# Performance work log

Hardware: AMD Instinct MI355X
Metric: run time of the kernel (lower is better)

## Reference

```python
import jax, jax.numpy as jnp
import numpy as np

NEG = float(-2**32 + 1)  # huge negative used by the original sign-based masking
EPS = 1e-8
NUM_BLOCKS = 3
NUM_HEADS = 1


def _mha(xq, xk, xv, Wq, bq, Wk, bk, Wv, bv):
    # manual QKV with ReLU, as in the torch module
    Q = jax.nn.relu(xq @ Wq + bq)   # [B, Lq, D]
    K = jax.nn.relu(xk @ Wk + bk)   # [B, Lk, D]
    V = jax.nn.relu(xv @ Wv + bv)
    B, Lq, D = Q.shape
    Lk = K.shape[1]
    dh = D // NUM_HEADS
    Qh = Q.reshape(B, Lq, NUM_HEADS, dh)
    Kh = K.reshape(B, Lk, NUM_HEADS, dh)
    Vh = V.reshape(B, Lk, NUM_HEADS, dh)
    scores = jnp.einsum('bqhd,bkhd->bhqk', Qh, Kh) / jnp.sqrt(jnp.float32(dh))
    # sign-based key padding mask (rows whose embedding-sum is exactly 0)
    key_mask0 = (jnp.sign(jnp.abs(jnp.sum(xk, axis=-1))) == 0.0).astype(scores.dtype)  # [B, Lk]
    cond = key_mask0[:, None, None, :]
    scores = NEG * cond + scores * (1.0 - cond)
    attn = jax.nn.softmax(scores, axis=-1)
    # post-softmax query mask
    qmask = jnp.sign(jnp.abs(jnp.sum(xq, axis=-1)))  # [B, Lq]
    attn = attn * qmask[:, None, :, None]
    out = jnp.einsum('bhqk,bkhd->bqhd', attn, Vh).reshape(B, Lq, D)
    return out + xq  # residual; note: the torch mha never applies its layernorm


def _layernorm(x, g, b):
    mu = jnp.mean(x, axis=-1, keepdims=True)
    var = jnp.mean(jnp.square(x - mu), axis=-1, keepdims=True)
    return (x - mu) / jnp.sqrt(var + EPS) * g + b


def _ffn(x, W1, b1, W2, b2, g, bln):
    h = jax.nn.relu(x @ W1 + b1) @ W2 + b2
    return _layernorm(h, g, bln) + x


def setup_inputs() -> dict:
    key = jax.random.key(0)
    ks = jax.random.split(key, 9)
    B, L, V, D, NB = 4096, 50, 50000, 200, NUM_BLOCKS
    tokens = jax.random.randint(ks[0], (B, L), 0, V)
    emb = jax.random.normal(ks[1], (V, D), dtype=jnp.float32) * 0.1
    emb = emb.at[0].set(0.0)  # padding token row -> triggers sign masks
    s = 1.0 / np.sqrt(D)
    Wq = jax.random.normal(ks[2], (NB, D, D), dtype=jnp.float32) * s
    Wk = jax.random.normal(ks[3], (NB, D, D), dtype=jnp.float32) * s
    Wv = jax.random.normal(ks[4], (NB, D, D), dtype=jnp.float32) * s
    W1 = jax.random.normal(ks[5], (NB, D, D), dtype=jnp.float32) * s
    W2 = jax.random.normal(ks[6], (NB, D, D), dtype=jnp.float32) * s
    z = jnp.zeros((NB, D), dtype=jnp.float32)
    return dict(tokens=tokens, emb=emb,
                Wq=Wq, bq=z, Wk=Wk, bk=z, Wv=Wv, bv=z,
                W1=W1, b1=z, W2=W2, b2=z,
                ln_g=jnp.ones((NB, D), dtype=jnp.float32), ln_b=z)


def reference(tokens, emb, Wq, bq, Wk, bk, Wv, bv, W1, b1, W2, b2, ln_g, ln_b):
    x = emb[tokens]  # [B, L, D]
    for i in range(NUM_BLOCKS):
        x = _mha(x, x, x, Wq[i], bq[i], Wk[i], bk[i], Wv[i], bv[i])
        x = _ffn(x, W1[i], b1[i], W2[i], b2[i], ln_g[i], ln_b[i])
    return x
```

## Files before the change

kernel.cpp:

```cpp
#include <hip/hip_runtime.h>
#include <hip/hip_bf16.h>
#include <math.h>

#define LQ 50
#define DD 200
#define NBLK 3
#define NT 512

#define KT 7
#define NTL 14
#define MAT_U (KT * NTL * 128)

#define APS 408
#define VTS 72
#define PS  136
#define SS  64

#define NEGC (-4294967295.0f)
#define SCALE 0.07071067811865475f

typedef __attribute__((ext_vector_type(4))) float f32x4;
typedef __attribute__((ext_vector_type(8))) short s16x8;

__device__ __forceinline__ unsigned short bf16_rne(float x) {
  unsigned u = __float_as_uint(x);
  unsigned r = u + 0x7FFF + ((u >> 16) & 1);
  return (unsigned short)(r >> 16);
}
__device__ __forceinline__ float bf16_f(unsigned short h) {
  return __uint_as_float((unsigned)h << 16);
}

__device__ __forceinline__ void splitf(float x, short& h, short& l) {
  __hip_bfloat16 bh = __float2bfloat16(x);
  float hf = __bfloat162float(bh);
  __hip_bfloat16 bl = __float2bfloat16(x - hf);
  h = (short)__builtin_bit_cast(unsigned short, bh);
  l = (short)__builtin_bit_cast(unsigned short, bl);
}
__device__ __forceinline__ unsigned short bfbits(float x) {
  __hip_bfloat16 bh = __float2bfloat16(x);
  return __builtin_bit_cast(unsigned short, bh);
}
__device__ __forceinline__ float joinf(short h, short l) {
  return __bfloat162float(__builtin_bit_cast(__hip_bfloat16, (unsigned short)h)) +
         __bfloat162float(__builtin_bit_cast(__hip_bfloat16, (unsigned short)l));
}

__device__ __forceinline__ float wave_sum(float v) {
  #pragma unroll
  for (int off = 32; off > 0; off >>= 1) v += __shfl_xor(v, off, 64);
  return v;
}
__device__ __forceinline__ float wave_max(float v) {
  #pragma unroll
  for (int off = 32; off > 0; off >>= 1) v = fmaxf(v, __shfl_xor(v, off, 64));
  return v;
}

__global__ __launch_bounds__(64)
void swizzle_w(const float* __restrict__ Wq, const float* __restrict__ Wk,
               const float* __restrict__ Wv, const float* __restrict__ W1,
               const float* __restrict__ W2, unsigned short* __restrict__ wbuf)
{
  int t = blockIdx.x;
  int nt = t % NTL; t /= NTL;
  int kt = t % KT;  t /= KT;
  int mat = t;
  int layer = mat / 5, which = mat % 5;
  const float* W;
  switch (which) {
    case 0: W = Wq; break;
    case 1: W = Wk; break;
    case 2: W = Wv; break;
    case 3: W = W1; break;
    default: W = W2; break;
  }
  W += (size_t)layer * DD * DD;

  const int l = threadIdx.x;
  const int g = l >> 4, c = l & 15;
  const int n = nt * 16 + c;
  s16x8 vh, vl;
  #pragma unroll
  for (int j = 0; j < 8; ++j) {
    int k = kt * 32 + g * 8 + j;
    float w = (k < DD && n < DD) ? W[k * DD + n] : 0.0f;
    unsigned short h = bf16_rne(w);
    unsigned short lo = bf16_rne(w - bf16_f(h));
    vh[j] = (short)h;
    vl[j] = (short)lo;
  }
  size_t base = ((size_t)(mat * KT * NTL + kt * NTL + nt) * 2) * 512 + l * 8;
  *(s16x8*)(wbuf + base)       = vh;
  *(s16x8*)(wbuf + base + 512) = vl;
}

template <int MODE>
__device__ __forceinline__ void big_matmul(
    const short* __restrict__ srcp, const s16x8* __restrict__ wt,
    const float* __restrict__ bias, short* __restrict__ dstp,
    float* __restrict__ dstf, int wv, int lane)
{
  const int g = lane >> 4, c = lane & 15;
  const int n1 = wv, n2 = wv + 8;
  const bool has2 = (n2 < 13);

  const short* arow[4];
  #pragma unroll
  for (int m = 0; m < 4; ++m) {
    int r = m * 16 + c;
    if (r >= LQ) r = 0;
    arow[m] = srcp + r * APS;
  }

  f32x4 acc0[4], acc1[4];
  #pragma unroll
  for (int m = 0; m < 4; ++m) { acc0[m] = (f32x4)0.f; acc1[m] = (f32x4)0.f; }

  const s16x8* p1 = wt + n1 * 128 + lane;
  s16x8 b1h = p1[0], b1l = p1[64];
  s16x8 b2h = (s16x8)0, b2l = (s16x8)0;
  if (has2) { const s16x8* p2 = wt + n2 * 128 + lane; b2h = p2[0]; b2l = p2[64]; }

  #pragma unroll 1
  for (int kt = 0; kt < KT; ++kt) {
    s16x8 x1h = (s16x8)0, x1l = (s16x8)0, x2h = (s16x8)0, x2l = (s16x8)0;
    if (kt + 1 < KT) {
      const s16x8* q1 = wt + ((kt + 1) * NTL + n1) * 128 + lane;
      x1h = q1[0]; x1l = q1[64];
      if (has2) {
        const s16x8* q2 = wt + ((kt + 1) * NTL + n2) * 128 + lane;
        x2h = q2[0]; x2l = q2[64];
      }
    }
    const int ch = kt * 4 + g;
    s16x8 ah[4], al[4];
    if (ch < 25) {
      #pragma unroll
      for (int m = 0; m < 4; ++m) {
        const short* ap = arow[m] + ch * 16;
        ah[m] = *(const s16x8*)ap;
        al[m] = *(const s16x8*)(ap + 8);
      }
    } else {
      #pragma unroll
      for (int m = 0; m < 4; ++m) { ah[m] = (s16x8)0; al[m] = (s16x8)0; }
    }
    #pragma unroll
    for (int m = 0; m < 4; ++m) {
      acc0[m] = __builtin_amdgcn_mfma_f32_16x16x32_bf16(ah[m], b1h, acc0[m], 0, 0, 0);
      acc0[m] = __builtin_amdgcn_mfma_f32_16x16x32_bf16(al[m], b1h, acc0[m], 0, 0, 0);
      acc0[m] = __builtin_amdgcn_mfma_f32_16x16x32_bf16(ah[m], b1l, acc0[m], 0, 0, 0);
    }
    if (has2) {
      #pragma unroll
      for (int m = 0; m < 4; ++m) {
        acc1[m] = __builtin_amdgcn_mfma_f32_16x16x32_bf16(ah[m], b2h, acc1[m], 0, 0, 0);
        acc1[m] = __builtin_amdgcn_mfma_f32_16x16x32_bf16(al[m], b2h, acc1[m], 0, 0, 0);
        acc1[m] = __builtin_amdgcn_mfma_f32_16x16x32_bf16(ah[m], b2l, acc1[m], 0, 0, 0);
      }
    }
    b1h = x1h; b1l = x1l; b2h = x2h; b2l = x2l;
  }

  #pragma unroll
  for (int t = 0; t < 2; ++t) {
    const int nt = t ? n2 : n1;
    const int col = nt * 16 + c;
    if (col < DD) {
      const float bv = bias[col];
      #pragma unroll
      for (int m = 0; m < 4; ++m) {
        const int rb = m * 16 + g * 4;
        if (MODE == 1) {
          float vv[4];
          #pragma unroll
          for (int q = 0; q < 4; ++q) {
            const int r = rb + q;
            float v = (t ? acc1[m][q] : acc0[m][q]) + bv;
            vv[q] = (r < LQ) ? fmaxf(v, 0.f) : 0.f;
          }
          unsigned u0 = (unsigned)bfbits(vv[0]) | ((unsigned)bfbits(vv[1]) << 16);
          unsigned u1 = (unsigned)bfbits(vv[2]) | ((unsigned)bfbits(vv[3]) << 16);
          uint2 pk; pk.x = u0; pk.y = u1;
          *(uint2*)(dstp + col * VTS + (rb >> 3) * 8 + (rb & 7)) = pk;
        } else {
          #pragma unroll
          for (int q = 0; q < 4; ++q) {
            const int r = rb + q;
            float v = (t ? acc1[m][q] : acc0[m][q]) + bv;
            if (MODE == 0) {
              if (r < LQ) {
                v = fmaxf(v, 0.f);
                short h, l; splitf(v, h, l);
                short* hp = dstp + r * APS + (col >> 3) * 16 + (col & 7);
                hp[0] = h; hp[8] = l;
              }
            } else {
              if (r < LQ) dstf[r * DD + col] = v;
            }
          }
        }
      }
    }
  }
}

__global__ __launch_bounds__(NT)
void transformer_kernel(const int* __restrict__ tokens,
                        const float* __restrict__ emb,
                        const unsigned short* __restrict__ wbuf,
                        const float* __restrict__ bq, const float* __restrict__ bk,
                        const float* __restrict__ bv, const float* __restrict__ b1,
                        const float* __restrict__ b2,
                        const float* __restrict__ lng, const float* __restrict__ lnb,
                        float* __restrict__ out)
{
  __shared__ __align__(16) short xs_p[LQ * APS];
  __shared__ __align__(16) short q_p [LQ * APS];
  __shared__ __align__(16) short k_p [LQ * APS];
  __shared__ __align__(16) short vt_p[DD * VTS];
  __shared__ float rowsum[52];

  float* Sf   = (float*)q_p;
  short* Pp   = q_p + 8192;
  float* aout = (float*)k_p;
  float* h2f  = (float*)k_p;

  const int b    = blockIdx.x;
  const int tid  = threadIdx.x;
  const int lane = tid & 63;
  const int wv   = tid >> 6;
  const int g    = lane >> 4, c = lane & 15;

  for (int o = tid; o < LQ * 25; o += NT) {
    int r = o / 25, ch = o % 25;
    int tok = tokens[b * LQ + r];
    const float* ep = emb + (size_t)tok * DD + ch * 8;
    float4 a0 = *(const float4*)ep;
    float4 a1 = *(const float4*)(ep + 4);
    float xv[8] = {a0.x, a0.y, a0.z, a0.w, a1.x, a1.y, a1.z, a1.w};
    s16x8 hh, ll;
    #pragma unroll
    for (int j = 0; j < 8; ++j) { short h, l; splitf(xv[j], h, l); hh[j] = h; ll[j] = l; }
    short* dp = xs_p + r * APS + ch * 16;
    *(s16x8*)dp = hh;
    *(s16x8*)(dp + 8) = ll;
  }
  __syncthreads();

  for (int layer = 0; layer < NBLK; ++layer) {
    const s16x8* wq  = (const s16x8*)wbuf + (size_t)(layer * 5 + 0) * MAT_U;
    const s16x8* wk  = (const s16x8*)wbuf + (size_t)(layer * 5 + 1) * MAT_U;
    const s16x8* wvv = (const s16x8*)wbuf + (size_t)(layer * 5 + 2) * MAT_U;
    const s16x8* w1  = (const s16x8*)wbuf + (size_t)(layer * 5 + 3) * MAT_U;
    const s16x8* w2  = (const s16x8*)wbuf + (size_t)(layer * 5 + 4) * MAT_U;
    const float* bql = bq + layer * DD;
    const float* bkl = bk + layer * DD;
    const float* bvl = bv + layer * DD;
    const float* b1l = b1 + layer * DD;
    const float* b2l = b2 + layer * DD;
    const float* gl  = lng + layer * DD;
    const float* bl  = lnb + layer * DD;

    for (int r = wv; r < LQ; r += 8) {
      float s = 0.f;
      #pragma unroll
      for (int t = 0; t < 4; ++t) {
        int cc = lane + 64 * t;
        if (cc < DD) {
          const short* p = xs_p + r * APS + (cc >> 3) * 16 + (cc & 7);
          s += joinf(p[0], p[8]);
        }
      }
      s = wave_sum(s);
      if (lane == 0) rowsum[r] = s;
    }

    big_matmul<0>(xs_p, wq,  bql, q_p,  nullptr, wv, lane);
    big_matmul<0>(xs_p, wk,  bkl, k_p,  nullptr, wv, lane);
    big_matmul<1>(xs_p, wvv, bvl, vt_p, nullptr, wv, lane);
    __syncthreads();

    f32x4 s0 = (f32x4)0.f, s1 = (f32x4)0.f;
    {
      const int mt = wv >> 1;
      const int nk0 = (wv & 1) * 2;
      int qr = mt * 16 + c;         if (qr >= LQ) qr = 0;
      int kj0 = nk0 * 16 + c;       if (kj0 >= LQ) kj0 = 0;
      int kj1 = (nk0 + 1) * 16 + c; if (kj1 >= LQ) kj1 = 0;
      const short* qrow = q_p + qr * APS;
      const short* k0r  = k_p + kj0 * APS;
      const short* k1r  = k_p + kj1 * APS;
      #pragma unroll 1
      for (int kt = 0; kt < KT; ++kt) {
        const int ch = kt * 4 + g;
        s16x8 qh = (s16x8)0, ql = (s16x8)0;
        s16x8 kh0 = (s16x8)0, kl0 = (s16x8)0, kh1 = (s16x8)0, kl1 = (s16x8)0;
        if (ch < 25) {
          qh  = *(const s16x8*)(qrow + ch * 16); ql  = *(const s16x8*)(qrow + ch * 16 + 8);
          kh0 = *(const s16x8*)(k0r + ch * 16);  kl0 = *(const s16x8*)(k0r + ch * 16 + 8);
          kh1 = *(const s16x8*)(k1r + ch * 16);  kl1 = *(const s16x8*)(k1r + ch * 16 + 8);
        }
        s0 = __builtin_amdgcn_mfma_f32_16x16x32_bf16(qh, kh0, s0, 0, 0, 0);
        s0 = __builtin_amdgcn_mfma_f32_16x16x32_bf16(ql, kh0, s0, 0, 0, 0);
        s0 = __builtin_amdgcn_mfma_f32_16x16x32_bf16(qh, kl0, s0, 0, 0, 0);
        s1 = __builtin_amdgcn_mfma_f32_16x16x32_bf16(qh, kh1, s1, 0, 0, 0);
        s1 = __builtin_amdgcn_mfma_f32_16x16x32_bf16(ql, kh1, s1, 0, 0, 0);
        s1 = __builtin_amdgcn_mfma_f32_16x16x32_bf16(qh, kl1, s1, 0, 0, 0);
      }
    }
    __syncthreads();

    {
      const int mt = wv >> 1;
      const int nk0 = (wv & 1) * 2;
      #pragma unroll
      for (int t = 0; t < 2; ++t) {
        const int j = (nk0 + t) * 16 + c;
        const f32x4 sa = t ? s1 : s0;
        const bool km = (j < LQ) && (rowsum[j] != 0.0f);
        #pragma unroll
        for (int q = 0; q < 4; ++q) {
          const int qi = mt * 16 + g * 4 + q;
          if (qi < LQ) Sf[qi * SS + j] = km ? sa[q] * SCALE : NEGC;
        }
      }
    }
    __syncthreads();

    for (int r = wv; r < LQ; r += 8) {
      float sm = -INFINITY;
      if (lane < LQ) sm = Sf[r * SS + lane];
      float m = wave_max(sm);
      float e = (lane < LQ) ? __expf(sm - m) : 0.0f;
      float ssum = wave_sum(e);
      float qm = (rowsum[r] == 0.0f) ? 0.0f : 1.0f;
      float a = e / ssum * qm;
      short h, l; splitf(a, h, l);
      short* pp = Pp + r * PS + (lane >> 3) * 16 + (lane & 7);
      pp[0] = h; pp[8] = l;
    }
    __syncthreads();

    {
      s16x8 pbh[4][2], pbl[4][2];
      #pragma unroll
      for (int nq = 0; nq < 4; ++nq) {
        int pr = nq * 16 + c; if (pr >= LQ) pr = 0;
        const short* pp = Pp + pr * PS;
        #pragma unroll
        for (int kt = 0; kt < 2; ++kt) {
          pbh[nq][kt] = *(const s16x8*)(pp + (kt * 4 + g) * 16);
          pbl[nq][kt] = *(const s16x8*)(pp + (kt * 4 + g) * 16 + 8);
        }
      }
      #pragma unroll
      for (int mi = 0; mi < 2; ++mi) {
        const int mt = wv + 8 * mi;
        if (mt < 13) {
          f32x4 pa[4];
          #pragma unroll
          for (int nq = 0; nq < 4; ++nq) pa[nq] = (f32x4)0.f;
          int vr = mt * 16 + c; if (vr >= DD) vr = 0;
          const short* vrow = vt_p + vr * VTS;
          #pragma unroll
          for (int kt = 0; kt < 2; ++kt) {
            s16x8 vh = *(const s16x8*)(vrow + (kt * 4 + g) * 8);
            #pragma unroll
            for (int nq = 0; nq < 4; ++nq) {
              pa[nq] = __builtin_amdgcn_mfma_f32_16x16x32_bf16(vh, pbh[nq][kt], pa[nq], 0, 0, 0);
              pa[nq] = __builtin_amdgcn_mfma_f32_16x16x32_bf16(vh, pbl[nq][kt], pa[nq], 0, 0, 0);
            }
          }
          const int d0 = mt * 16 + g * 4;
          if (d0 + 3 < DD) {
            #pragma unroll
            for (int nq = 0; nq < 4; ++nq) {
              const int qq = nq * 16 + c;
              if (qq < LQ) {
                float4 w4; w4.x = pa[nq][0]; w4.y = pa[nq][1];
                w4.z = pa[nq][2]; w4.w = pa[nq][3];
                *(float4*)(aout + qq * 200 + d0) = w4;
              }
            }
          }
        }
      }
    }
    __syncthreads();

    for (int o = tid; o < LQ * 25; o += NT) {
      int r = o / 25, ch = o % 25;
      const float* ap = aout + r * 200 + ch * 8;
      float4 a0 = *(const float4*)ap;
      float4 a1 = *(const float4*)(ap + 4);
      float av[8] = {a0.x, a0.y, a0.z, a0.w, a1.x, a1.y, a1.z, a1.w};
      short* xp = xs_p + r * APS + ch * 16;
      s16x8 hh = *(const s16x8*)xp;
      s16x8 ll = *(const s16x8*)(xp + 8);
      #pragma unroll
      for (int j = 0; j < 8; ++j) {
        float f = joinf(hh[j], ll[j]) + av[j];
        short h, l; splitf(f, h, l);
        hh[j] = h; ll[j] = l;
      }
      *(s16x8*)xp = hh;
      *(s16x8*)(xp + 8) = ll;
    }
    __syncthreads();

    big_matmul<0>(xs_p, w1, b1l, q_p, nullptr, wv, lane);
    __syncthreads();
    big_matmul<2>(q_p, w2, b2l, nullptr, h2f, wv, lane);
    __syncthreads();

    for (int r = wv; r < LQ; r += 8) {
      float hv[4];
      #pragma unroll
      for (int t = 0; t < 4; ++t) {
        int cc = lane + 64 * t;
        hv[t] = (cc < DD) ? h2f[r * DD + cc] : 0.f;
      }
      float mu = wave_sum(hv[0] + hv[1] + hv[2] + hv[3]) * (1.0f / 200.0f);
      float d0 = hv[0] - mu, d1 = hv[1] - mu, d2 = hv[2] - mu;
      float d3 = (lane + 192 < DD) ? (hv[3] - mu) : 0.f;
      float var = wave_sum(d0 * d0 + d1 * d1 + d2 * d2 + d3 * d3) * (1.0f / 200.0f);
      float inv = 1.0f / sqrtf(var + 1e-8f);
      float dd4[4] = {d0, d1, d2, d3};
      #pragma unroll
      for (int t = 0; t < 4; ++t) {
        int cc = lane + 64 * t;
        if (cc < DD) {
          short* hp = xs_p + r * APS + (cc >> 3) * 16 + (cc & 7);
          float nv = dd4[t] * inv * gl[cc] + bl[cc] + joinf(hp[0], hp[8]);
          short h, l; splitf(nv, h, l);
          hp[0] = h; hp[8] = l;
        }
      }
    }
    __syncthreads();
  }

  for (int o = tid; o < LQ * 25; o += NT) {
    int r = o / 25, ch = o % 25;
    const short* sp = xs_p + r * APS + ch * 16;
    s16x8 hh = *(const s16x8*)sp;
    s16x8 ll = *(const s16x8*)(sp + 8);
    float4 o0, o1;
    o0.x = joinf(hh[0], ll[0]); o0.y = joinf(hh[1], ll[1]);
    o0.z = joinf(hh[2], ll[2]); o0.w = joinf(hh[3], ll[3]);
    o1.x = joinf(hh[4], ll[4]); o1.y = joinf(hh[5], ll[5]);
    o1.z = joinf(hh[6], ll[6]); o1.w = joinf(hh[7], ll[7]);
    float* op = out + ((size_t)b * LQ + r) * DD + ch * 8;
    *(float4*)op = o0;
    *(float4*)(op + 4) = o1;
  }
}

extern "C" void kernel_launch(void* const* d_in, const int* in_sizes, int n_in,
                              void* d_out, int out_size, void* d_ws, size_t ws_size,
                              hipStream_t stream) {
  const int*   tokens = (const int*)  d_in[0];
  const float* emb    = (const float*)d_in[1];
  const float* Wq     = (const float*)d_in[2];
  const float* bq     = (const float*)d_in[3];
  const float* Wk     = (const float*)d_in[4];
  const float* bk     = (const float*)d_in[5];
  const float* Wv     = (const float*)d_in[6];
  const float* bv     = (const float*)d_in[7];
  const float* W1     = (const float*)d_in[8];
  const float* b1     = (const float*)d_in[9];
  const float* W2     = (const float*)d_in[10];
  const float* b2     = (const float*)d_in[11];
  const float* lng    = (const float*)d_in[12];
  const float* lnb    = (const float*)d_in[13];
  float* out = (float*)d_out;
  unsigned short* wbuf = (unsigned short*)d_ws;

  hipLaunchKernelGGL(swizzle_w, dim3(15 * KT * NTL), dim3(64), 0, stream,
                     Wq, Wk, Wv, W1, W2, wbuf);

  const int B = in_sizes[0] / LQ;
  hipLaunchKernelGGL(transformer_kernel, dim3(B), dim3(NT), 0, stream,
                     tokens, emb, wbuf, bq, bk, bv, b1, b2, lng, lnb, out);
}
```

Measured before the change: 1.887 ms.

## Fuse attention residual into PV epilogue and transpose MODE0 MFMA for vector stores

The attention output is no longer staged as fp32 in shared memory and added to x in a separate pass. The PV epilogue now reads the split bf16 hi/lo x values, adds the MFMA result and writes the result back in place, which removes one full pass and one barrier. The MODE 0 matmul swaps its MFMA operands so each lane holds four consecutive columns, letting the epilogue use packed 8-byte stores. SS is padded from 64 to 66, likely to reduce LDS bank conflicts, at the cost of extra code paths and more careful aliasing with xs_p.

```diff
diff --git a/kernel.cpp b/kernel.cpp
--- a/kernel.cpp
+++ b/kernel.cpp
@@ -14,7 +14,7 @@
 #define APS 408
 #define VTS 72
 #define PS  136
-#define SS  64
+#define SS  66
 
 #define NEGC (-4294967295.0f)
 #define SCALE 0.07071067811865475f
@@ -147,57 +147,100 @@
       #pragma unroll
       for (int m = 0; m < 4; ++m) { ah[m] = (s16x8)0; al[m] = (s16x8)0; }
     }
+    if (MODE == 0) {
+      #pragma unroll
+      for (int m = 0; m < 4; ++m) {
+        acc0[m] = __builtin_amdgcn_mfma_f32_16x16x32_bf16(b1h, ah[m], acc0[m], 0, 0, 0);
+        acc0[m] = __builtin_amdgcn_mfma_f32_16x16x32_bf16(b1h, al[m], acc0[m], 0, 0, 0);
+        acc0[m] = __builtin_amdgcn_mfma_f32_16x16x32_bf16(b1l, ah[m], acc0[m], 0, 0, 0);
+      }
+      if (has2) {
+        #pragma unroll
+        for (int m = 0; m < 4; ++m) {
+          acc1[m] = __builtin_amdgcn_mfma_f32_16x16x32_bf16(b2h, ah[m], acc1[m], 0, 0, 0);
+          acc1[m] = __builtin_amdgcn_mfma_f32_16x16x32_bf16(b2h, al[m], acc1[m], 0, 0, 0);
+          acc1[m] = __builtin_amdgcn_mfma_f32_16x16x32_bf16(b2l, ah[m], acc1[m], 0, 0, 0);
+        }
+      }
+    } else {
+      #pragma unroll
+      for (int m = 0; m < 4; ++m) {
+        acc0[m] = __builtin_amdgcn_mfma_f32_16x16x32_bf16(ah[m], b1h, acc0[m], 0, 0, 0);
+        acc0[m] = __builtin_amdgcn_mfma_f32_16x16x32_bf16(al[m], b1h, acc0[m], 0, 0, 0);
+        acc0[m] = __builtin_amdgcn_mfma_f32_16x16x32_bf16(ah[m], b1l, acc0[m], 0, 0, 0);
+      }
+      if (has2) {
+        #pragma unroll
+        for (int m = 0; m < 4; ++m) {
+          acc1[m] = __builtin_amdgcn_mfma_f32_16x16x32_bf16(ah[m], b2h, acc1[m], 0, 0, 0);
+          acc1[m] = __builtin_amdgcn_mfma_f32_16x16x32_bf16(al[m], b2h, acc1[m], 0, 0, 0);
+          acc1[m] = __builtin_amdgcn_mfma_f32_16x16x32_bf16(ah[m], b2l, acc1[m], 0, 0, 0);
+        }
+      }
+    }
+    b1h = x1h; b1l = x1l; b2h = x2h; b2l = x2l;
+  }
+
+  if (MODE == 0) {
     #pragma unroll
-    for (int m = 0; m < 4; ++m) {
-      acc0[m] = __builtin_amdgcn_mfma_f32_16x16x32_bf16(ah[m], b1h, acc0[m], 0, 0, 0);
-      acc0[m] = __builtin_amdgcn_mfma_f32_16x16x32_bf16(al[m], b1h, acc0[m], 0, 0, 0);
-      acc0[m] = __builtin_amdgcn_mfma_f32_16x16x32_bf16(ah[m], b1l, acc0[m], 0, 0, 0);
-    }
-    if (has2) {
-      #pragma unroll
-      for (int m = 0; m < 4; ++m) {
-        acc1[m] = __builtin_amdgcn_mfma_f32_16x16x32_bf16(ah[m], b2h, acc1[m], 0, 0, 0);
-        acc1[m] = __builtin_amdgcn_mfma_f32_16x16x32_bf16(al[m], b2h, acc1[m], 0, 0, 0);
-        acc1[m] = __builtin_amdgcn_mfma_f32_16x16x32_bf16(ah[m], b2l, acc1[m], 0, 0, 0);
-      }
-    }
-    b1h = x1h; b1l = x1l; b2h = x2h; b2l = x2l;
-  }
-
-  #pragma unroll
-  for (int t = 0; t < 2; ++t) {
-    const int nt = t ? n2 : n1;
-    const int col = nt * 16 + c;
-    if (col < DD) {
-      const float bv = bias[col];
-      #pragma unroll
-      for (int m = 0; m < 4; ++m) {
-        const int rb = m * 16 + g * 4;
-        if (MODE == 1) {
-          float vv[4];
+    for (int t = 0; t < 2; ++t) {
+      const int nt = t ? n2 : n1;
+      if (nt < 13) {
+        const int nb = nt * 16 + g * 4;
+        if (nb + 3 < DD) {
+          float4 bv = *(const float4*)(bias + nb);
           #pragma unroll
-          for (int q = 0; q < 4; ++q) {
-            const int r = rb + q;
-            float v = (t ? acc1[m][q] : acc0[m][q]) + bv;
-            vv[q] = (r < LQ) ? fmaxf(v, 0.f) : 0.f;
+          for (int m = 0; m < 4; ++m) {
+            const int r = m * 16 + c;
+            if (r < LQ) {
+              const f32x4 ac = t ? acc1[m] : acc0[m];
+              float v0 = fmaxf(ac[0] + bv.x, 0.f);
+              float v1 = fmaxf(ac[1] + bv.y, 0.f);
+              float v2 = fmaxf(ac[2] + bv.z, 0.f);
+              float v3 = fmaxf(ac[3] + bv.w, 0.f);
+              short h0, l0, h1, l1, h2, l2, h3, l3;
+              splitf(v0, h0, l0); splitf(v1, h1, l1);
+              splitf(v2, h2, l2); splitf(v3, h3, l3);
+              uint2 ph, pl;
+              ph.x = (unsigned short)h0 | ((unsigned)(unsigned short)h1 << 16);
+              ph.y = (unsigned short)h2 | ((unsigned)(unsigned short)h3 << 16);
+              pl.x = (unsigned short)l0 | ((unsigned)(unsigned short)l1 << 16);
+              pl.y = (unsigned short)l2 | ((unsigned)(unsigned short)l3 << 16);
+              short* base = dstp + r * APS + (nb >> 3) * 16 + (nb & 7);
+              *(uint2*)base = ph;
+              *(uint2*)(base + 8) = pl;
+            }
           }
-          unsigned u0 = (unsigned)bfbits(vv[0]) | ((unsigned)bfbits(vv[1]) << 16);
-          unsigned u1 = (unsigned)bfbits(vv[2]) | ((unsigned)bfbits(vv[3]) << 16);
-          uint2 pk; pk.x = u0; pk.y = u1;
-          *(uint2*)(dstp + col * VTS + (rb >> 3) * 8 + (rb & 7)) = pk;
-        } else {
-          #pragma unroll
-          for (int q = 0; q < 4; ++q) {
-            const int r = rb + q;
-            float v = (t ? acc1[m][q] : acc0[m][q]) + bv;
-            if (MODE == 0) {
-              if (r < LQ) {
-                v = fmaxf(v, 0.f);
-                short h, l; splitf(v, h, l);
-                short* hp = dstp + r * APS + (col >> 3) * 16 + (col & 7);
-                hp[0] = h; hp[8] = l;
-              }
-            } else {
+        }
+      }
+    }
+  } else {
+    #pragma unroll
+    for (int t = 0; t < 2; ++t) {
+      const int nt = t ? n2 : n1;
+      const int col = nt * 16 + c;
+      if (col < DD) {
+        const float bv = bias[col];
+        #pragma unroll
+        for (int m = 0; m < 4; ++m) {
+          const int rb = m * 16 + g * 4;
+          if (MODE == 1) {
+            float vv[4];
+            #pragma unroll
+            for (int q = 0; q < 4; ++q) {
+              const int r = rb + q;
+              float v = (t ? acc1[m][q] : acc0[m][q]) + bv;
+              vv[q] = (r < LQ) ? fmaxf(v, 0.f) : 0.f;
+            }
+            unsigned u0 = (unsigned)bfbits(vv[0]) | ((unsigned)bfbits(vv[1]) << 16);
+            unsigned u1 = (unsigned)bfbits(vv[2]) | ((unsigned)bfbits(vv[3]) << 16);
+            uint2 pk; pk.x = u0; pk.y = u1;
+            *(uint2*)(dstp + col * VTS + (rb >> 3) * 8 + (rb & 7)) = pk;
+          } else {
+            #pragma unroll
+            for (int q = 0; q < 4; ++q) {
+              const int r = rb + q;
+              float v = (t ? acc1[m][q] : acc0[m][q]) + bv;
               if (r < LQ) dstf[r * DD + col] = v;
             }
           }
@@ -225,7 +268,6 @@
 
   float* Sf   = (float*)q_p;
   short* Pp   = q_p + 8192;
-  float* aout = (float*)k_p;
   float* h2f  = (float*)k_p;
 
   const int b    = blockIdx.x;
@@ -380,34 +422,27 @@
             for (int nq = 0; nq < 4; ++nq) {
               const int qq = nq * 16 + c;
               if (qq < LQ) {
-                float4 w4; w4.x = pa[nq][0]; w4.y = pa[nq][1];
-                w4.z = pa[nq][2]; w4.w = pa[nq][3];
-                *(float4*)(aout + qq * 200 + d0) = w4;
+                short* base = xs_p + qq * APS + (d0 >> 3) * 16 + (d0 & 7);
+                uint2 ph = *(const uint2*)base;
+                uint2 pl = *(const uint2*)(base + 8);
+                float f0 = joinf((short)(ph.x & 0xFFFF), (short)(pl.x & 0xFFFF)) + pa[nq][0];
+                float f1 = joinf((short)(ph.x >> 16),    (short)(pl.x >> 16))    + pa[nq][1];
+                float f2 = joinf((short)(ph.y & 0xFFFF), (short)(pl.y & 0xFFFF)) + pa[nq][2];
+                float f3 = joinf((short)(ph.y >> 16),    (short)(pl.y >> 16))    + pa[nq][3];
+                short h0, l0, h1, l1, h2, l2, h3, l3;
+                splitf(f0, h0, l0); splitf(f1, h1, l1);
+                splitf(f2, h2, l2); splitf(f3, h3, l3);
+                ph.x = (unsigned short)h0 | ((unsigned)(unsigned short)h1 << 16);
+                ph.y = (unsigned short)h2 | ((unsigned)(unsigned short)h3 << 16);
+                pl.x = (unsigned short)l0 | ((unsigned)(unsigned short)l1 << 16);
+                pl.y = (unsigned short)l2 | ((unsigned)(unsigned short)l3 << 16);
+                *(uint2*)base = ph;
+                *(uint2*)(base + 8) = pl;
               }
             }
           }
         }
       }
-    }
-    __syncthreads();
-
-    for (int o = tid; o < LQ * 25; o += NT) {
-      int r = o / 25, ch = o % 25;
-      const float* ap = aout + r * 200 + ch * 8;
-      float4 a0 = *(const float4*)ap;
-      float4 a1 = *(const float4*)(ap + 4);
-      float av[8] = {a0.x, a0.y, a0.z, a0.w, a1.x, a1.y, a1.z, a1.w};
-      short* xp = xs_p + r * APS + ch * 16;
-      s16x8 hh = *(const s16x8*)xp;
-      s16x8 ll = *(const s16x8*)(xp + 8);
-      #pragma unroll
-      for (int j = 0; j < 8; ++j) {
-        float f = joinf(hh[j], ll[j]) + av[j];
-        short h, l; splitf(f, h, l);
-        hh[j] = h; ll[j] = l;
-      }
-      *(s16x8*)xp = hh;
-      *(s16x8*)(xp + 8) = ll;
     }
     __syncthreads();
 
```

Result: no change. 1.887 ms (+0.0%).
